# Kernel tuning notes

Hardware: AMD Instinct MI355X
Metric: run time of the kernel (lower is better)

Reference implementation:

```python
import jax, jax.numpy as jnp
import numpy as np

D_MODEL = 768
D_POS = 64
NHEAD = 12
D_FF = 3072
HEAD_DIM = D_MODEL // NHEAD
LN_EPS = 1e-5


def _layer_norm(x, gamma, beta):
    mu = jnp.mean(x, axis=-1, keepdims=True)
    var = jnp.var(x, axis=-1, keepdims=True)
    return (x - mu) * jax.lax.rsqrt(var + LN_EPS) * gamma + beta


def setup_inputs() -> dict:
    key = jax.random.key(0)
    ks = jax.random.split(key, 16)
    L, N = 256, 4
    s = 0.02
    return {
        "src": jax.random.normal(ks[0], (L, N, D_MODEL), jnp.float32),
        "pos": jax.random.normal(ks[1], (N, L, L, D_POS), jnp.float32),
        "q_w": jax.random.normal(ks[2], (D_MODEL, D_MODEL), jnp.float32) * s,
        "q_b": jnp.zeros((D_MODEL,), jnp.float32),
        "k_w": jax.random.normal(ks[3], (D_MODEL, D_MODEL), jnp.float32) * s,
        "k_b": jnp.zeros((D_MODEL,), jnp.float32),
        "v_w": jax.random.normal(ks[4], (D_MODEL, D_MODEL), jnp.float32) * s,
        "v_b": jnp.zeros((D_MODEL,), jnp.float32),
        "p_w": jax.random.normal(ks[5], (D_MODEL, D_POS), jnp.float32) * s,
        "p_b": jnp.zeros((D_MODEL,), jnp.float32),
        "out_w": jax.random.normal(ks[6], (D_MODEL, D_MODEL), jnp.float32) * s,
        "out_b": jnp.zeros((D_MODEL,), jnp.float32),
        "lin1_w": jax.random.normal(ks[7], (D_FF, D_MODEL), jnp.float32) * s,
        "lin1_b": jnp.zeros((D_FF,), jnp.float32),
        "lin2_w": jax.random.normal(ks[8], (D_MODEL, D_FF), jnp.float32) * s,
        "lin2_b": jnp.zeros((D_MODEL,), jnp.float32),
        "n1_g": jnp.ones((D_MODEL,), jnp.float32),
        "n1_b": jnp.zeros((D_MODEL,), jnp.float32),
        "n2_g": jnp.ones((D_MODEL,), jnp.float32),
        "n2_b": jnp.zeros((D_MODEL,), jnp.float32),
    }


def reference(src, pos, q_w, q_b, k_w, k_b, v_w, v_b, p_w, p_b,
              out_w, out_b, lin1_w, lin1_b, lin2_w, lin2_b,
              n1_g, n1_b, n2_g, n2_b):
    L, N, E = src.shape
    H, hd = NHEAD, HEAD_DIM
    scaling = float(hd) ** -0.5

    # projections (F.linear: x @ W.T + b)
    q = (src @ q_w.T + q_b).reshape(L, N, H, hd).transpose(1, 2, 0, 3) * scaling  # (N,H,L,hd)
    k = (src @ k_w.T + k_b).reshape(L, N, H, hd).transpose(1, 2, 0, 3)            # (N,H,L,hd)
    v = (src @ v_w.T + v_b).reshape(L, N, H, hd).transpose(1, 2, 0, 3)            # (N,H,L,hd)
    p = (pos @ p_w.T + p_b).reshape(N, L, L, H, hd)                               # (N,L,L,H,hd)

    # content-content + content-position scores
    scores = jnp.einsum('nhid,nhjd->nhij', q, k) \
           + jnp.einsum('nhid,nijhd->nhij', q, p)                                 # (N,H,L,L)
    attn = jax.nn.softmax(scores, axis=-1)

    ctx = jnp.einsum('nhij,nhjd->nhid', attn, v)          # (N,H,L,hd)
    ctx = ctx.transpose(2, 0, 1, 3).reshape(L, N, E)      # (L,N,E)
    attn_out = ctx @ out_w.T + out_b

    x = _layer_norm(src + attn_out, n1_g, n1_b)
    ff = jax.nn.gelu(x @ lin1_w.T + lin1_b, approximate=False) @ lin2_w.T + lin2_b
    x = _layer_norm(x + ff, n2_g, n2_b)
    return x
```

## Files before the change

kernel.cpp:

```cpp
#include <hip/hip_runtime.h>
#include <hip/hip_bf16.h>
#include <math.h>

typedef __hip_bfloat16 bf16;
typedef unsigned short u16;
typedef __attribute__((ext_vector_type(8))) short bf16x8;
typedef __attribute__((ext_vector_type(4))) float f32x4;

#define L_SEQ 256
#define NB 4
#define EMB 768
#define NH 12
#define DFF 3072
#define HD 64

__device__ __forceinline__ float ldE(const void* p, size_t i, int f32) {
    return f32 ? ((const float*)p)[i] : __bfloat162float(((const bf16*)p)[i]);
}
__device__ __forceinline__ float b2f(u16 v) { return __uint_as_float(((unsigned)v) << 16); }
__device__ __forceinline__ u16 f2b(float v) {
    bf16 h = __float2bfloat16(v);
    return *(u16*)&h;
}

__device__ __forceinline__ void cvt8(u16* dst, const void* s, size_t off, int f32) {
    if (f32) {
        const float* sf = (const float*)s + off;
        #pragma unroll
        for (int t = 0; t < 8; ++t) dst[t] = f2b(sf[t]);
    } else {
        *(uint4*)dst = *(const uint4*)((const u16*)s + off);
    }
}

__global__ void pack_all(u16* __restrict__ xb, u16* __restrict__ wqkv,
                         u16* __restrict__ owb, u16* __restrict__ l1b,
                         u16* __restrict__ l2b, float* __restrict__ biasf,
                         u16* __restrict__ p_wT,
                         const void* src, const void* qw, const void* kw, const void* vw,
                         const void* ow, const void* l1w, const void* l2w,
                         const void* qb, const void* kb, const void* vb,
                         const void* ob, const void* b1, const void* b2,
                         const void* pw, const void* pb,
                         int* __restrict__ flagp) {
    __shared__ int cnt[256];
    int t = threadIdx.x;
    {
        unsigned w = ((const unsigned*)src)[t];
        unsigned e = ((w & 0xFFFFu) >> 7) & 0xFFu;
        cnt[t] = (e >= 0xC3u) ? 1 : 0;
        __syncthreads();
        for (int off = 128; off; off >>= 1) {
            if (t < off) cnt[t] += cnt[t + off];
            __syncthreads();
        }
    }
    const int f32 = (cnt[0] > 8) ? 1 : 0;
    int b = blockIdx.x;
    if (b == 0 && t == 0) *flagp = f32;
    if (b >= 3867) {
        int o = (b - 3867) * 256 + t;
        if (o >= 6240) return;
        int idx = o * 8;
        int c = idx / EMB, e0 = idx % EMB;
        u16 tmp[8];
        if (c < 64) {
            #pragma unroll
            for (int k = 0; k < 8; ++k) tmp[k] = f2b(ldE(pw, (size_t)(e0 + k) * 64 + c, f32));
        } else {
            #pragma unroll
            for (int k = 0; k < 8; ++k) tmp[k] = f2b(ldE(pb, e0 + k, f32));
        }
        *(uint4*)(p_wT + idx) = *(uint4*)tmp;
        return;
    }
    if (b >= 3840) {
        int o = (b - 3840) * 256 + t;
        if (o >= 6912) return;
        float v;
        if (o < 768)       v = ldE(qb, o, f32);
        else if (o < 1536) v = ldE(kb, o - 768, f32);
        else if (o < 2304) v = ldE(vb, o - 1536, f32);
        else if (o < 3072) v = ldE(ob, o - 2304, f32);
        else if (o < 6144) v = ldE(b1, o - 3072, f32);
        else               v = ldE(b2, o - 6144, f32);
        biasf[o] = v;
        return;
    }
    int gid = b * 256 + t;
    u16 tmp[8];
    if (gid < 98304) {
        size_t idx = (size_t)gid * 8;
        cvt8(tmp, src, idx, f32);
        *(uint4*)(xb + idx) = *(uint4*)tmp;
    } else if (gid < 319488) {
        size_t idx = (size_t)(gid - 98304) * 8;
        int r = (int)(idx / EMB);
        const void* s;
        size_t off;
        if (r < EMB)          { s = qw; off = idx; }
        else if (r < 2 * EMB) { s = kw; off = idx - (size_t)EMB * EMB; }
        else                  { s = vw; off = idx - (size_t)2 * EMB * EMB; }
        cvt8(tmp, s, off, f32);
        *(uint4*)(wqkv + idx) = *(uint4*)tmp;
    } else if (gid < 393216) {
        size_t idx = (size_t)(gid - 319488) * 8;
        cvt8(tmp, ow, idx, f32);
        *(uint4*)(owb + idx) = *(uint4*)tmp;
    } else if (gid < 688128) {
        size_t idx = (size_t)(gid - 393216) * 8;
        cvt8(tmp, l1w, idx, f32);
        *(uint4*)(l1b + idx) = *(uint4*)tmp;
    } else {
        size_t idx = (size_t)(gid - 688128) * 8;
        cvt8(tmp, l2w, idx, f32);
        *(uint4*)(l2b + idx) = *(uint4*)tmp;
    }
}

template <int MODE>
__global__ __launch_bounds__(256) void mfma_gemm(
        const u16* __restrict__ A, const u16* __restrict__ W,
        const float* __restrict__ biasf,
        u16* __restrict__ outB0, u16* __restrict__ outB1, u16* __restrict__ outB2,
        float* __restrict__ outF, float* __restrict__ outF2,
        int K, int lda, int ksplit) {
    __shared__ u16 As[128][40];
    __shared__ u16 Ws[128][40];
    int tid = threadIdx.x;
    int wave = tid >> 6, lane = tid & 63;
    int quad = lane >> 4, col = lane & 15;
    int m0 = blockIdx.y * 128, n0 = blockIdx.x * 128;
    int z = blockIdx.z;
    const u16* Ap = A + (size_t)z * ksplit;
    const u16* Wp = W + (size_t)z * ksplit;
    int wm = (wave >> 1) * 64, wn = (wave & 1) * 64;
    f32x4 acc[4][4];
    #pragma unroll
    for (int a = 0; a < 4; ++a)
        #pragma unroll
        for (int b = 0; b < 4; ++b) acc[a][b] = (f32x4){0.f, 0.f, 0.f, 0.f};
    for (int k0 = 0; k0 < K; k0 += 32) {
        #pragma unroll
        for (int it = 0; it < 2; ++it) {
            int l = tid + it * 256;
            int r = l >> 2, c4 = (l & 3) * 8;
            *(uint4*)&As[r][c4] = *(const uint4*)&Ap[(size_t)(m0 + r) * lda + k0 + c4];
            *(uint4*)&Ws[r][c4] = *(const uint4*)&Wp[(size_t)(n0 + r) * lda + k0 + c4];
        }
        __syncthreads();
        bf16x8 af[4], bfr[4];
        #pragma unroll
        for (int mi = 0; mi < 4; ++mi)
            af[mi] = __builtin_bit_cast(bf16x8, *(const uint4*)&As[wm + mi * 16 + col][quad * 8]);
        #pragma unroll
        for (int ni = 0; ni < 4; ++ni)
            bfr[ni] = __builtin_bit_cast(bf16x8, *(const uint4*)&Ws[wn + ni * 16 + col][quad * 8]);
        #pragma unroll
        for (int mi = 0; mi < 4; ++mi)
            #pragma unroll
            for (int ni = 0; ni < 4; ++ni)
                acc[mi][ni] = __builtin_amdgcn_mfma_f32_16x16x32_bf16(
                    af[mi], bfr[ni], acc[mi][ni], 0, 0, 0);
        __syncthreads();
    }
    #pragma unroll
    for (int mi = 0; mi < 4; ++mi)
        #pragma unroll
        for (int ni = 0; ni < 4; ++ni)
            #pragma unroll
            for (int reg = 0; reg < 4; ++reg) {
                int rr = m0 + wm + mi * 16 + quad * 4 + reg;
                int cc = n0 + wn + ni * 16 + col;
                float v = acc[mi][ni][reg];
                if (MODE == 0) {
                    v += biasf[cc];
                    if (cc < EMB) {
                        outB0[(size_t)rr * EMB + cc] = f2b(v * 0.125f);
                    } else if (cc < 2 * EMB) {
                        outB1[(size_t)rr * EMB + cc - EMB] = f2b(v);
                    } else {
                        outB2[((size_t)(rr & 3) * EMB + (cc - 2 * EMB)) * L_SEQ + (rr >> 2)] = f2b(v);
                    }
                } else if (MODE == 2) {
                    v += biasf[cc];
                    v = 0.5f * v * (1.0f + erff(v * 0.70710678118654752f));
                    outB0[(size_t)rr * DFF + cc] = f2b(v);
                } else if (MODE == 4) {
                    float* o = z ? outF2 : outF;
                    o[(size_t)rr * EMB + cc] = v;
                } else {
                    atomicAdd(&outF[(size_t)rr * EMB + cc], v);
                }
            }
}

__global__ __launch_bounds__(256) void s2q_mfma(
        const u16* __restrict__ qbp, const u16* __restrict__ p_wT,
        const void* __restrict__ pos, float* __restrict__ S,
        const int* __restrict__ flagp) {
    const int f32 = *flagp;
    __shared__ u16 qp_l[4][16][68];
    __shared__ float qpb_l[4][16];
    int wave = threadIdx.x >> 6, lane = threadIdx.x & 63;
    int quad = lane >> 4, col = lane & 15;
    int wid = (blockIdx.x << 2) + wave;
    int i = wid & 255, n = wid >> 8;
    const u16* qrow = qbp + (size_t)(i * NB + n) * EMB;

    f32x4 qpacc[5];
    #pragma unroll
    for (int nt = 0; nt < 5; ++nt) qpacc[nt] = (f32x4){0.f, 0.f, 0.f, 0.f};
    #pragma unroll
    for (int kt = 0; kt < 24; ++kt) {
        int owner = (4 * kt + quad) >> 3;
        uint4 av = (col == owner) ? *(const uint4*)(qrow + kt * 32 + quad * 8)
                                  : (uint4){0u, 0u, 0u, 0u};
        bf16x8 a = __builtin_bit_cast(bf16x8, av);
        #pragma unroll
        for (int nt = 0; nt < 5; ++nt) {
            bf16x8 bb = __builtin_bit_cast(bf16x8,
                *(const uint4*)(p_wT + (size_t)(nt * 16 + col) * EMB + kt * 32 + quad * 8));
            qpacc[nt] = __builtin_amdgcn_mfma_f32_16x16x32_bf16(a, bb, qpacc[nt], 0, 0, 0);
        }
    }
    #pragma unroll
    for (int nt = 0; nt < 4; ++nt)
        #pragma unroll
        for (int reg = 0; reg < 4; ++reg)
            qp_l[wave][quad * 4 + reg][nt * 16 + col] = f2b(qpacc[nt][reg]);
    if (col == 0) {
        #pragma unroll
        for (int reg = 0; reg < 4; ++reg) qpb_l[wave][quad * 4 + reg] = qpacc[4][reg];
    }
    bf16x8 a0 = __builtin_bit_cast(bf16x8, *(const uint4*)&qp_l[wave][col][quad * 8]);
    bf16x8 a1 = __builtin_bit_cast(bf16x8, *(const uint4*)&qp_l[wave][col][32 + quad * 8]);
    float qpb_r[4];
    #pragma unroll
    for (int reg = 0; reg < 4; ++reg) qpb_r[reg] = qpb_l[wave][quad * 4 + reg];

    #pragma unroll 4
    for (int t = 0; t < 16; ++t) {
        int j = t * 16 + col;
        size_t pbase = ((size_t)(n * L_SEQ + i) * L_SEQ + j) * HD;
        bf16x8 b0, b1;
        if (f32) {
            const float* pf = (const float*)pos + pbase;
            u16 tmp[16];
            #pragma unroll
            for (int c = 0; c < 8; ++c) tmp[c] = f2b(pf[quad * 8 + c]);
            #pragma unroll
            for (int c = 0; c < 8; ++c) tmp[8 + c] = f2b(pf[32 + quad * 8 + c]);
            b0 = *(bf16x8*)tmp;
            b1 = *(bf16x8*)(tmp + 8);
        } else {
            const u16* pb = (const u16*)pos + pbase;
            b0 = __builtin_bit_cast(bf16x8, *(const uint4*)(pb + quad * 8));
            b1 = __builtin_bit_cast(bf16x8, *(const uint4*)(pb + 32 + quad * 8));
        }
        f32x4 acc = (f32x4){0.f, 0.f, 0.f, 0.f};
        acc = __builtin_amdgcn_mfma_f32_16x16x32_bf16(a0, b0, acc, 0, 0, 0);
        acc = __builtin_amdgcn_mfma_f32_16x16x32_bf16(a1, b1, acc, 0, 0, 0);
        if (quad < 3) {
            #pragma unroll
            for (int reg = 0; reg < 4; ++reg) {
                int h = quad * 4 + reg;
                S[(((size_t)n * NH + h) * L_SEQ + i) * L_SEQ + j] = acc[reg] + qpb_r[reg];
            }
        }
    }
}

__global__ __launch_bounds__(128) void attn3_kernel(
        const u16* __restrict__ qb, const u16* __restrict__ kb,
        const u16* __restrict__ vt, const float* __restrict__ S,
        u16* __restrict__ ctxb) {
    __shared__ u16 p_lds[2][16][268];
    int b = blockIdx.x;
    int n = b / 96, rem = b % 96, h = rem >> 3, it = rem & 7;
    int wave = threadIdx.x >> 6, lane = threadIdx.x & 63;
    int quad = lane >> 4, col = lane & 15;
    int i0 = it * 32 + wave * 16;

    const u16* qrow = qb + ((size_t)(i0 + col) * NB + n) * EMB + h * HD;
    bf16x8 a0 = __builtin_bit_cast(bf16x8, *(const uint4*)(qrow + quad * 8));
    bf16x8 a1 = __builtin_bit_cast(bf16x8, *(const uint4*)(qrow + 32 + quad * 8));

    f32x4 sc[16];
    #pragma unroll
    for (int t = 0; t < 16; ++t) {
        const u16* krow = kb + ((size_t)(t * 16 + col) * NB + n) * EMB + h * HD;
        bf16x8 b0 = __builtin_bit_cast(bf16x8, *(const uint4*)(krow + quad * 8));
        bf16x8 b1 = __builtin_bit_cast(bf16x8, *(const uint4*)(krow + 32 + quad * 8));
        f32x4 acc = (f32x4){0.f, 0.f, 0.f, 0.f};
        acc = __builtin_amdgcn_mfma_f32_16x16x32_bf16(a0, b0, acc, 0, 0, 0);
        acc = __builtin_amdgcn_mfma_f32_16x16x32_bf16(a1, b1, acc, 0, 0, 0);
        sc[t] = acc;
    }

    #pragma unroll
    for (int reg = 0; reg < 4; ++reg) {
        const float* Srow = S + (((size_t)n * NH + h) * L_SEQ + i0 + quad * 4 + reg) * L_SEQ + col;
        float m = -1e30f;
        #pragma unroll
        for (int t = 0; t < 16; ++t) {
            float v = sc[t][reg] + Srow[t * 16];
            sc[t][reg] = v;
            m = fmaxf(m, v);
        }
        #pragma unroll
        for (int off = 1; off < 16; off <<= 1) m = fmaxf(m, __shfl_xor(m, off));
        float sum = 0.f;
        #pragma unroll
        for (int t = 0; t < 16; ++t) {
            float e = __expf(sc[t][reg] - m);
            sc[t][reg] = e;
            sum += e;
        }
        #pragma unroll
        for (int off = 1; off < 16; off <<= 1) sum += __shfl_xor(sum, off);
        float inv = 1.0f / sum;
        #pragma unroll
        for (int t = 0; t < 16; ++t)
            p_lds[wave][quad * 4 + reg][t * 16 + col] = f2b(sc[t][reg] * inv);
    }

    bf16x8 ap[8];
    #pragma unroll
    for (int kt = 0; kt < 8; ++kt)
        ap[kt] = __builtin_bit_cast(bf16x8, *(const uint4*)&p_lds[wave][col][kt * 32 + quad * 8]);
    #pragma unroll
    for (int nt = 0; nt < 4; ++nt) {
        const u16* vrow = vt + ((size_t)n * EMB + h * HD + nt * 16 + col) * L_SEQ;
        f32x4 acc = (f32x4){0.f, 0.f, 0.f, 0.f};
        #pragma unroll
        for (int kt = 0; kt < 8; ++kt) {
            bf16x8 bp = __builtin_bit_cast(bf16x8, *(const uint4*)(vrow + kt * 32 + quad * 8));
            acc = __builtin_amdgcn_mfma_f32_16x16x32_bf16(ap[kt], bp, acc, 0, 0, 0);
        }
        #pragma unroll
        for (int reg = 0; reg < 4; ++reg) {
            int ii = i0 + quad * 4 + reg;
            ctxb[((size_t)ii * NB + n) * EMB + h * HD + nt * 16 + col] = f2b(acc[reg]);
        }
    }
}

__global__ void ln1_kernel(const float* __restrict__ p0, const float* __restrict__ p1,
                           const void* __restrict__ src, const float* __restrict__ biasf,
                           const void* __restrict__ g, const void* __restrict__ b,
                           u16* __restrict__ x1b, float* __restrict__ y2,
                           const int* __restrict__ flagp) {
    const int f32 = *flagp;
    int r = blockIdx.x;
    int t = threadIdx.x;
    __shared__ float red[256];
    float x[3];
    #pragma unroll
    for (int p = 0; p < 3; ++p) {
        int e = t + p * 256;
        size_t oi = (size_t)r * EMB + e;
        x[p] = p0[oi] + p1[oi] + ldE(src, oi, f32) + biasf[2304 + e];
    }
    red[t] = x[0] + x[1] + x[2];
    __syncthreads();
    for (int off = 128; off; off >>= 1) {
        if (t < off) red[t] += red[t + off];
        __syncthreads();
    }
    float mean = red[0] * (1.0f / EMB);
    __syncthreads();
    float d0 = x[0] - mean, d1 = x[1] - mean, d2 = x[2] - mean;
    red[t] = d0 * d0 + d1 * d1 + d2 * d2;
    __syncthreads();
    for (int off = 128; off; off >>= 1) {
        if (t < off) red[t] += red[t + off];
        __syncthreads();
    }
    float rstd = rsqrtf(red[0] * (1.0f / EMB) + 1e-5f);
    float vs[3] = {d0, d1, d2};
    #pragma unroll
    for (int p = 0; p < 3; ++p) {
        int e = t + p * 256;
        float v = vs[p] * rstd * ldE(g, e, f32) + ldE(b, e, f32);
        size_t oi = (size_t)r * EMB + e;
        x1b[oi] = f2b(v);
        y2[oi] = v + biasf[6144 + e];
    }
}

__global__ void ln2_kernel(const float* __restrict__ X, const void* __restrict__ g,
                           const void* __restrict__ b, void* __restrict__ outAny,
                           const int* __restrict__ flagp) {
    const int f32 = *flagp;
    int r = blockIdx.x;
    int t = threadIdx.x;
    __shared__ float red[256];
    float x0 = X[(size_t)r * EMB + t];
    float x1 = X[(size_t)r * EMB + t + 256];
    float x2 = X[(size_t)r * EMB + t + 512];
    red[t] = x0 + x1 + x2;
    __syncthreads();
    for (int off = 128; off; off >>= 1) {
        if (t < off) red[t] += red[t + off];
        __syncthreads();
    }
    float mean = red[0] * (1.0f / EMB);
    __syncthreads();
    float d0 = x0 - mean, d1 = x1 - mean, d2 = x2 - mean;
    red[t] = d0 * d0 + d1 * d1 + d2 * d2;
    __syncthreads();
    for (int off = 128; off; off >>= 1) {
        if (t < off) red[t] += red[t + off];
        __syncthreads();
    }
    float rstd = rsqrtf(red[0] * (1.0f / EMB) + 1e-5f);
    float vs[3] = {d0, d1, d2};
    #pragma unroll
    for (int p = 0; p < 3; ++p) {
        int e = t + p * 256;
        float v = vs[p] * rstd * ldE(g, e, f32) + ldE(b, e, f32);
        size_t oi = (size_t)r * EMB + e;
        if (f32) ((float*)outAny)[oi] = v;
        else     ((bf16*)outAny)[oi] = __float2bfloat16(v);
    }
}

extern "C" void kernel_launch(void* const* d_in, const int* in_sizes, int n_in,
                              void* d_out, int out_size, void* d_ws, size_t ws_size,
                              hipStream_t stream) {
    const void* src    = d_in[0];
    const void* pos    = d_in[1];
    const void* q_w    = d_in[2];
    const void* q_b    = d_in[3];
    const void* k_w    = d_in[4];
    const void* k_b    = d_in[5];
    const void* v_w    = d_in[6];
    const void* v_b    = d_in[7];
    const void* p_w    = d_in[8];
    const void* p_b    = d_in[9];
    const void* out_w  = d_in[10];
    const void* out_b  = d_in[11];
    const void* lin1_w = d_in[12];
    const void* lin1_b = d_in[13];
    const void* lin2_w = d_in[14];
    const void* lin2_b = d_in[15];
    const void* n1_g   = d_in[16];
    const void* n1_b   = d_in[17];
    const void* n2_g   = d_in[18];
    const void* n2_b   = d_in[19];

    float* f = (float*)d_ws;
    int*   flagp = (int*)f;
    float* biasf = f + 16;
    u16*   xb    = (u16*)(f + 6928);
    u16*   wqkv  = (u16*)(f + 400144);
    u16*   owb   = (u16*)(f + 1284880);
    u16*   l1b   = (u16*)(f + 1579792);
    u16*   l2b   = (u16*)(f + 2759440);
    u16*   qbp   = (u16*)(f + 3939088);
    u16*   kbp   = (u16*)(f + 4332304);
    u16*   vtb   = (u16*)(f + 4725520);
    u16*   p_wT  = (u16*)(f + 5118736);
    float* S     = f + 5143824;
    u16*   ctxb  = (u16*)(f + 8289552);
    u16*   ffb   = (u16*)S;
    float* y2    = S + 1572864;
    float* pOut1 = S + 2359296;
    float* pOut0 = f + 400144;
    u16*   x1b   = vtb;

    pack_all<<<3892, 256, 0, stream>>>(xb, wqkv, owb, l1b, l2b, biasf, p_wT,
                                       src, q_w, k_w, v_w, out_w, lin1_w, lin2_w,
                                       q_b, k_b, v_b, out_b, lin1_b, lin2_b,
                                       p_w, p_b, flagp);

    mfma_gemm<0><<<dim3(18, 8), 256, 0, stream>>>(
        xb, wqkv, biasf, qbp, kbp, vtb, nullptr, nullptr, EMB, EMB, 0);

    s2q_mfma<<<NB * L_SEQ / 4, 256, 0, stream>>>(qbp, p_wT, pos, S, flagp);

    attn3_kernel<<<NB * NH * 8, 128, 0, stream>>>(qbp, kbp, vtb, S, ctxb);

    mfma_gemm<4><<<dim3(6, 8, 2), 256, 0, stream>>>(
        ctxb, owb, nullptr, nullptr, nullptr, nullptr, pOut0, pOut1, 384, EMB, 384);

    ln1_kernel<<<1024, 256, 0, stream>>>(pOut0, pOut1, src, biasf, n1_g, n1_b,
                                         x1b, y2, flagp);

    mfma_gemm<2><<<dim3(24, 8), 256, 0, stream>>>(
        x1b, l1b, biasf + 3072, ffb, nullptr, nullptr, nullptr, nullptr, EMB, EMB, 0);

    mfma_gemm<5><<<dim3(6, 8, 4), 256, 0, stream>>>(
        ffb, l2b, nullptr, nullptr, nullptr, nullptr, y2, nullptr, 768, DFF, 768);

    ln2_kernel<<<1024, 256, 0, stream>>>(y2, n2_g, n2_b, d_out, flagp);
}
```

Measured before the change: 316.0 us.

## Fuse fp32-to-bf16 conversion into GEMM tile loads and batch pos loads in s2q

Removes the large pack kernel that converted src and all weight matrices to bf16 in workspace. The GEMMs now read the original inputs directly and convert each tile to bf16 while staging it into shared memory, and biases are read straight from the inputs. This drops a full pass over the weights and its extra kernel launch. The cost is redundant conversion work in every GEMM block that reads the same tile, plus float loads twice as wide. The s2q kernel's bf16 path now issues 8 pos loads ahead of the MFMAs to increase memory-level parallelism, but that path only runs for bf16 inputs; the fp32 inputs in this test take the unchanged fp32 branch.

After: 411.8 us. 30.3% more time.

```diff
diff --git a/kernel.cpp b/kernel.cpp
--- a/kernel.cpp
+++ b/kernel.cpp
@@ -23,108 +23,60 @@
     return *(u16*)&h;
 }
 
-__device__ __forceinline__ void cvt8(u16* dst, const void* s, size_t off, int f32) {
+__device__ __forceinline__ void stage8(u16* dst, const void* s, size_t off, int f32) {
     if (f32) {
         const float* sf = (const float*)s + off;
-        #pragma unroll
-        for (int t = 0; t < 8; ++t) dst[t] = f2b(sf[t]);
+        float4 a = *(const float4*)sf;
+        float4 b = *(const float4*)(sf + 4);
+        u16 t[8] = {f2b(a.x), f2b(a.y), f2b(a.z), f2b(a.w),
+                    f2b(b.x), f2b(b.y), f2b(b.z), f2b(b.w)};
+        *(uint4*)dst = *(uint4*)t;
     } else {
         *(uint4*)dst = *(const uint4*)((const u16*)s + off);
     }
 }
 
-__global__ void pack_all(u16* __restrict__ xb, u16* __restrict__ wqkv,
-                         u16* __restrict__ owb, u16* __restrict__ l1b,
-                         u16* __restrict__ l2b, float* __restrict__ biasf,
-                         u16* __restrict__ p_wT,
-                         const void* src, const void* qw, const void* kw, const void* vw,
-                         const void* ow, const void* l1w, const void* l2w,
-                         const void* qb, const void* kb, const void* vb,
-                         const void* ob, const void* b1, const void* b2,
-                         const void* pw, const void* pb,
-                         int* __restrict__ flagp) {
+__global__ void pack_small(u16* __restrict__ p_wT, const void* __restrict__ src,
+                           const void* __restrict__ pw, const void* __restrict__ pb,
+                           int* __restrict__ flagp) {
     __shared__ int cnt[256];
     int t = threadIdx.x;
-    {
-        unsigned w = ((const unsigned*)src)[t];
-        unsigned e = ((w & 0xFFFFu) >> 7) & 0xFFu;
-        cnt[t] = (e >= 0xC3u) ? 1 : 0;
-        __syncthreads();
-        for (int off = 128; off; off >>= 1) {
-            if (t < off) cnt[t] += cnt[t + off];
-            __syncthreads();
-        }
+    unsigned w = ((const unsigned*)src)[t];
+    unsigned e = ((w & 0xFFFFu) >> 7) & 0xFFu;
+    cnt[t] = (e >= 0xC3u) ? 1 : 0;
+    __syncthreads();
+    for (int off = 128; off; off >>= 1) {
+        if (t < off) cnt[t] += cnt[t + off];
+        __syncthreads();
     }
     const int f32 = (cnt[0] > 8) ? 1 : 0;
-    int b = blockIdx.x;
-    if (b == 0 && t == 0) *flagp = f32;
-    if (b >= 3867) {
-        int o = (b - 3867) * 256 + t;
-        if (o >= 6240) return;
-        int idx = o * 8;
-        int c = idx / EMB, e0 = idx % EMB;
-        u16 tmp[8];
-        if (c < 64) {
-            #pragma unroll
-            for (int k = 0; k < 8; ++k) tmp[k] = f2b(ldE(pw, (size_t)(e0 + k) * 64 + c, f32));
-        } else {
-            #pragma unroll
-            for (int k = 0; k < 8; ++k) tmp[k] = f2b(ldE(pb, e0 + k, f32));
-        }
-        *(uint4*)(p_wT + idx) = *(uint4*)tmp;
-        return;
-    }
-    if (b >= 3840) {
-        int o = (b - 3840) * 256 + t;
-        if (o >= 6912) return;
-        float v;
-        if (o < 768)       v = ldE(qb, o, f32);
-        else if (o < 1536) v = ldE(kb, o - 768, f32);
-        else if (o < 2304) v = ldE(vb, o - 1536, f32);
-        else if (o < 3072) v = ldE(ob, o - 2304, f32);
-        else if (o < 6144) v = ldE(b1, o - 3072, f32);
-        else               v = ldE(b2, o - 6144, f32);
-        biasf[o] = v;
-        return;
-    }
-    int gid = b * 256 + t;
+    if (blockIdx.x == 0 && t == 0) *flagp = f32;
+    int o = blockIdx.x * 256 + t;
+    if (o >= 6240) return;
+    int idx = o * 8;
+    int c = idx / EMB, e0 = idx % EMB;
     u16 tmp[8];
-    if (gid < 98304) {
-        size_t idx = (size_t)gid * 8;
-        cvt8(tmp, src, idx, f32);
-        *(uint4*)(xb + idx) = *(uint4*)tmp;
-    } else if (gid < 319488) {
-        size_t idx = (size_t)(gid - 98304) * 8;
-        int r = (int)(idx / EMB);
-        const void* s;
-        size_t off;
-        if (r < EMB)          { s = qw; off = idx; }
-        else if (r < 2 * EMB) { s = kw; off = idx - (size_t)EMB * EMB; }
-        else                  { s = vw; off = idx - (size_t)2 * EMB * EMB; }
-        cvt8(tmp, s, off, f32);
-        *(uint4*)(wqkv + idx) = *(uint4*)tmp;
-    } else if (gid < 393216) {
-        size_t idx = (size_t)(gid - 319488) * 8;
-        cvt8(tmp, ow, idx, f32);
-        *(uint4*)(owb + idx) = *(uint4*)tmp;
-    } else if (gid < 688128) {
-        size_t idx = (size_t)(gid - 393216) * 8;
-        cvt8(tmp, l1w, idx, f32);
-        *(uint4*)(l1b + idx) = *(uint4*)tmp;
+    if (c < 64) {
+        #pragma unroll
+        for (int k = 0; k < 8; ++k) tmp[k] = f2b(ldE(pw, (size_t)(e0 + k) * 64 + c, f32));
     } else {
-        size_t idx = (size_t)(gid - 688128) * 8;
-        cvt8(tmp, l2w, idx, f32);
-        *(uint4*)(l2b + idx) = *(uint4*)tmp;
-    }
-}
-
-template <int MODE>
+        #pragma unroll
+        for (int k = 0; k < 8; ++k) tmp[k] = f2b(ldE(pb, e0 + k, f32));
+    }
+    *(uint4*)(p_wT + idx) = *(uint4*)tmp;
+}
+
+template <int MODE, int AEXT>
 __global__ __launch_bounds__(256) void mfma_gemm(
-        const u16* __restrict__ A, const u16* __restrict__ W,
-        const float* __restrict__ biasf,
+        const void* __restrict__ A, const void* __restrict__ W0,
+        const void* __restrict__ W1, const void* __restrict__ W2,
+        const void* __restrict__ b0, const void* __restrict__ b1,
+        const void* __restrict__ b2,
         u16* __restrict__ outB0, u16* __restrict__ outB1, u16* __restrict__ outB2,
         float* __restrict__ outF, float* __restrict__ outF2,
-        int K, int lda, int ksplit) {
+        int K, int lda, int ksplit, const int* __restrict__ flagp) {
+    const int f32 = *flagp;
+    const int af32 = AEXT ? f32 : 0;
     __shared__ u16 As[128][40];
     __shared__ u16 Ws[128][40];
     int tid = threadIdx.x;
@@ -132,8 +84,14 @@
     int quad = lane >> 4, col = lane & 15;
     int m0 = blockIdx.y * 128, n0 = blockIdx.x * 128;
     int z = blockIdx.z;
-    const u16* Ap = A + (size_t)z * ksplit;
-    const u16* Wp = W + (size_t)z * ksplit;
+    size_t zoff = (size_t)z * ksplit;
+    const void* Wt = W0;
+    int nb = n0, sel = 0;
+    if (MODE == 0) {
+        sel = n0 / EMB;
+        Wt = sel == 0 ? W0 : (sel == 1 ? W1 : W2);
+        nb = n0 - sel * EMB;
+    }
     int wm = (wave >> 1) * 64, wn = (wave & 1) * 64;
     f32x4 acc[4][4];
     #pragma unroll
@@ -145,8 +103,8 @@
         for (int it = 0; it < 2; ++it) {
             int l = tid + it * 256;
             int r = l >> 2, c4 = (l & 3) * 8;
-            *(uint4*)&As[r][c4] = *(const uint4*)&Ap[(size_t)(m0 + r) * lda + k0 + c4];
-            *(uint4*)&Ws[r][c4] = *(const uint4*)&Wp[(size_t)(n0 + r) * lda + k0 + c4];
+            stage8(&As[r][c4], A, (size_t)(m0 + r) * lda + k0 + c4 + zoff, af32);
+            stage8(&Ws[r][c4], Wt, (size_t)(nb + r) * lda + k0 + c4 + zoff, f32);
         }
         __syncthreads();
         bf16x8 af[4], bfr[4];
@@ -174,16 +132,18 @@
                 int cc = n0 + wn + ni * 16 + col;
                 float v = acc[mi][ni][reg];
                 if (MODE == 0) {
-                    v += biasf[cc];
-                    if (cc < EMB) {
-                        outB0[(size_t)rr * EMB + cc] = f2b(v * 0.125f);
-                    } else if (cc < 2 * EMB) {
-                        outB1[(size_t)rr * EMB + cc - EMB] = f2b(v);
+                    int cl = cc - sel * EMB;
+                    const void* bt = sel == 0 ? b0 : (sel == 1 ? b1 : b2);
+                    v += ldE(bt, cl, f32);
+                    if (sel == 0) {
+                        outB0[(size_t)rr * EMB + cl] = f2b(v * 0.125f);
+                    } else if (sel == 1) {
+                        outB1[(size_t)rr * EMB + cl] = f2b(v);
                     } else {
-                        outB2[((size_t)(rr & 3) * EMB + (cc - 2 * EMB)) * L_SEQ + (rr >> 2)] = f2b(v);
+                        outB2[((size_t)(rr & 3) * EMB + cl) * L_SEQ + (rr >> 2)] = f2b(v);
                     }
                 } else if (MODE == 2) {
-                    v += biasf[cc];
+                    v += ldE(b0, cc, f32);
                     v = 0.5f * v * (1.0f + erff(v * 0.70710678118654752f));
                     outB0[(size_t)rr * DFF + cc] = f2b(v);
                 } else if (MODE == 4) {
@@ -239,33 +199,54 @@
     #pragma unroll
     for (int reg = 0; reg < 4; ++reg) qpb_r[reg] = qpb_l[wave][quad * 4 + reg];
 
-    #pragma unroll 4
-    for (int t = 0; t < 16; ++t) {
-        int j = t * 16 + col;
-        size_t pbase = ((size_t)(n * L_SEQ + i) * L_SEQ + j) * HD;
-        bf16x8 b0, b1;
-        if (f32) {
-            const float* pf = (const float*)pos + pbase;
+    size_t rowbase = ((size_t)(n * L_SEQ + i) * L_SEQ) * HD;
+    if (!f32) {
+        #pragma unroll
+        for (int g = 0; g < 2; ++g) {
+            uint4 r0[8], r1[8];
+            #pragma unroll
+            for (int t8 = 0; t8 < 8; ++t8) {
+                int j = (g * 8 + t8) * 16 + col;
+                const u16* pb = (const u16*)pos + rowbase + (size_t)j * HD;
+                r0[t8] = *(const uint4*)(pb + quad * 8);
+                r1[t8] = *(const uint4*)(pb + 32 + quad * 8);
+            }
+            #pragma unroll
+            for (int t8 = 0; t8 < 8; ++t8) {
+                int j = (g * 8 + t8) * 16 + col;
+                f32x4 acc = (f32x4){0.f, 0.f, 0.f, 0.f};
+                acc = __builtin_amdgcn_mfma_f32_16x16x32_bf16(
+                    a0, __builtin_bit_cast(bf16x8, r0[t8]), acc, 0, 0, 0);
+                acc = __builtin_amdgcn_mfma_f32_16x16x32_bf16(
+                    a1, __builtin_bit_cast(bf16x8, r1[t8]), acc, 0, 0, 0);
+                if (quad < 3) {
+                    #pragma unroll
+                    for (int reg = 0; reg < 4; ++reg) {
+                        int h = quad * 4 + reg;
+                        S[(((size_t)n * NH + h) * L_SEQ + i) * L_SEQ + j] = acc[reg] + qpb_r[reg];
+                    }
+                }
+            }
+        }
+    } else {
+        #pragma unroll 4
+        for (int t = 0; t < 16; ++t) {
+            int j = t * 16 + col;
+            const float* pf = (const float*)pos + rowbase + (size_t)j * HD;
             u16 tmp[16];
             #pragma unroll
             for (int c = 0; c < 8; ++c) tmp[c] = f2b(pf[quad * 8 + c]);
             #pragma unroll
             for (int c = 0; c < 8; ++c) tmp[8 + c] = f2b(pf[32 + quad * 8 + c]);
-            b0 = *(bf16x8*)tmp;
-            b1 = *(bf16x8*)(tmp + 8);
-        } else {
-            const u16* pb = (const u16*)pos + pbase;
-            b0 = __builtin_bit_cast(bf16x8, *(const uint4*)(pb + quad * 8));
-            b1 = __builtin_bit_cast(bf16x8, *(const uint4*)(pb + 32 + quad * 8));
-        }
-        f32x4 acc = (f32x4){0.f, 0.f, 0.f, 0.f};
-        acc = __builtin_amdgcn_mfma_f32_16x16x32_bf16(a0, b0, acc, 0, 0, 0);
-        acc = __builtin_amdgcn_mfma_f32_16x16x32_bf16(a1, b1, acc, 0, 0, 0);
-        if (quad < 3) {
-            #pragma unroll
-            for (int reg = 0; reg < 4; ++reg) {
-                int h = quad * 4 + reg;
-                S[(((size_t)n * NH + h) * L_SEQ + i) * L_SEQ + j] = acc[reg] + qpb_r[reg];
+            f32x4 acc = (f32x4){0.f, 0.f, 0.f, 0.f};
+            acc = __builtin_amdgcn_mfma_f32_16x16x32_bf16(a0, *(bf16x8*)tmp, acc, 0, 0, 0);
+            acc = __builtin_amdgcn_mfma_f32_16x16x32_bf16(a1, *(bf16x8*)(tmp + 8), acc, 0, 0, 0);
+            if (quad < 3) {
+                #pragma unroll
+                for (int reg = 0; reg < 4; ++reg) {
+                    int h = quad * 4 + reg;
+                    S[(((size_t)n * NH + h) * L_SEQ + i) * L_SEQ + j] = acc[reg] + qpb_r[reg];
+                }
             }
         }
     }
@@ -347,7 +328,8 @@
 }
 
 __global__ void ln1_kernel(const float* __restrict__ p0, const float* __restrict__ p1,
-                           const void* __restrict__ src, const float* __restrict__ biasf,
+                           const void* __restrict__ src, const void* __restrict__ out_b,
+                           const void* __restrict__ lin2_b,
                            const void* __restrict__ g, const void* __restrict__ b,
                            u16* __restrict__ x1b, float* __restrict__ y2,
                            const int* __restrict__ flagp) {
@@ -360,7 +342,7 @@
     for (int p = 0; p < 3; ++p) {
         int e = t + p * 256;
         size_t oi = (size_t)r * EMB + e;
-        x[p] = p0[oi] + p1[oi] + ldE(src, oi, f32) + biasf[2304 + e];
+        x[p] = p0[oi] + p1[oi] + ldE(src, oi, f32) + ldE(out_b, e, f32);
     }
     red[t] = x[0] + x[1] + x[2];
     __syncthreads();
@@ -385,7 +367,7 @@
         float v = vs[p] * rstd * ldE(g, e, f32) + ldE(b, e, f32);
         size_t oi = (size_t)r * EMB + e;
         x1b[oi] = f2b(v);
-        y2[oi] = v + biasf[6144 + e];
+        y2[oi] = v + ldE(lin2_b, e, f32);
     }
 }
 
@@ -452,47 +434,42 @@
 
     float* f = (float*)d_ws;
     int*   flagp = (int*)f;
-    float* biasf = f + 16;
-    u16*   xb    = (u16*)(f + 6928);
-    u16*   wqkv  = (u16*)(f + 400144);
-    u16*   owb   = (u16*)(f + 1284880);
-    u16*   l1b   = (u16*)(f + 1579792);
-    u16*   l2b   = (u16*)(f + 2759440);
-    u16*   qbp   = (u16*)(f + 3939088);
-    u16*   kbp   = (u16*)(f + 4332304);
-    u16*   vtb   = (u16*)(f + 4725520);
-    u16*   p_wT  = (u16*)(f + 5118736);
-    float* S     = f + 5143824;
-    u16*   ctxb  = (u16*)(f + 8289552);
+    u16*   p_wT  = (u16*)(f + 16);
+    u16*   qbp   = (u16*)(f + 24976);
+    u16*   kbp   = (u16*)(f + 418192);
+    u16*   vtb   = (u16*)(f + 811408);
+    float* S     = f + 1204624;
+    u16*   ctxb  = (u16*)(f + 4350352);
+    float* pOut0 = f + 4743568;
     u16*   ffb   = (u16*)S;
     float* y2    = S + 1572864;
     float* pOut1 = S + 2359296;
-    float* pOut0 = f + 400144;
     u16*   x1b   = vtb;
 
-    pack_all<<<3892, 256, 0, stream>>>(xb, wqkv, owb, l1b, l2b, biasf, p_wT,
-                                       src, q_w, k_w, v_w, out_w, lin1_w, lin2_w,
-                                       q_b, k_b, v_b, out_b, lin1_b, lin2_b,
-                                       p_w, p_b, flagp);
-
-    mfma_gemm<0><<<dim3(18, 8), 256, 0, stream>>>(
-        xb, wqkv, biasf, qbp, kbp, vtb, nullptr, nullptr, EMB, EMB, 0);
+    pack_small<<<25, 256, 0, stream>>>(p_wT, src, p_w, p_b, flagp);
+
+    mfma_gemm<0, 1><<<dim3(18, 8), 256, 0, stream>>>(
+        src, q_w, k_w, v_w, q_b, k_b, v_b, qbp, kbp, vtb, nullptr, nullptr,
+        EMB, EMB, 0, flagp);
 
     s2q_mfma<<<NB * L_SEQ / 4, 256, 0, stream>>>(qbp, p_wT, pos, S, flagp);
 
     attn3_kernel<<<NB * NH * 8, 128, 0, stream>>>(qbp, kbp, vtb, S, ctxb);
 
-    mfma_gemm<4><<<dim3(6, 8, 2), 256, 0, stream>>>(
-        ctxb, owb, nullptr, nullptr, nullptr, nullptr, pOut0, pOut1, 384, EMB, 384);
-
-    ln1_kernel<<<1024, 256, 0, stream>>>(pOut0, pOut1, src, biasf, n1_g, n1_b,
-                                         x1b, y2, flagp);
-
-    mfma_gemm<2><<<dim3(24, 8), 256, 0, stream>>>(
-        x1b, l1b, biasf + 3072, ffb, nullptr, nullptr, nullptr, nullptr, EMB, EMB, 0);
-
-    mfma_gemm<5><<<dim3(6, 8, 4), 256, 0, stream>>>(
-        ffb, l2b, nullptr, nullptr, nullptr, nullptr, y2, nullptr, 768, DFF, 768);
+    mfma_gemm<4, 0><<<dim3(6, 8, 2), 256, 0, stream>>>(
+        ctxb, out_w, nullptr, nullptr, nullptr, nullptr, nullptr,
+        nullptr, nullptr, nullptr, pOut0, pOut1, 384, EMB, 384, flagp);
+
+    ln1_kernel<<<1024, 256, 0, stream>>>(pOut0, pOut1, src, out_b, lin2_b,
+                                         n1_g, n1_b, x1b, y2, flagp);
+
+    mfma_gemm<2, 0><<<dim3(24, 8), 256, 0, stream>>>(
+        x1b, lin1_w, nullptr, nullptr, lin1_b, nullptr, nullptr,
+        ffb, nullptr, nullptr, nullptr, nullptr, EMB, EMB, 0, flagp);
+
+    mfma_gemm<5, 0><<<dim3(6, 8, 4), 256, 0, stream>>>(
+        ffb, lin2_w, nullptr, nullptr, nullptr, nullptr, nullptr,
+        nullptr, nullptr, nullptr, y2, nullptr, 768, DFF, 768, flagp);
 
     ln2_kernel<<<1024, 256, 0, stream>>>(y2, n2_g, n2_b, d_out, flagp);
 }
```
